# Performance work log

Measured on AMD Instinct MI355X. Metric: run time of the kernel, lower is better.

## Reference

```python
import jax, jax.numpy as jnp
import numpy as np

D = 512  # feature_dim


def setup_inputs() -> dict:
    key = jax.random.key(0)
    ks = jax.random.split(key, 10)
    s = 1.0 / np.sqrt(D)
    s2 = 1.0 / np.sqrt(2 * D)
    return {
        "X": jax.random.normal(ks[0], (8, 2048, D), dtype=jnp.float32),
        "Y": jax.random.normal(ks[1], (8, 2048, D), dtype=jnp.float32),
        "W_xq": jax.random.uniform(ks[2], (D, D), jnp.float32, -s, s),
        "b_xq": jax.random.uniform(ks[3], (D,), jnp.float32, -s, s),
        "W_yq": jax.random.uniform(ks[4], (D, D), jnp.float32, -s, s),
        "b_yq": jax.random.uniform(ks[5], (D,), jnp.float32, -s, s),
        "W_fk": jax.random.uniform(ks[6], (D, 2 * D), jnp.float32, -s2, s2),
        "b_fk": jax.random.uniform(ks[7], (D,), jnp.float32, -s2, s2),
        "W_fv": jax.random.uniform(ks[8], (D, 2 * D), jnp.float32, -s2, s2),
        "b_fv": jax.random.uniform(ks[9], (D,), jnp.float32, -s2, s2),
    }


def reference(X, Y, W_xq, b_xq, W_yq, b_yq, W_fk, b_fk, W_fv, b_fv):
    # Dropout is evaluated in eval mode (identity).
    scale = 1.0 / jnp.sqrt(jnp.asarray(D, X.dtype))
    Q1 = jnp.einsum('bsd,ed->bse', X, W_xq) + b_xq  # [B,S,D]
    Q2 = jnp.einsum('bsd,ed->bse', Y, W_yq) + b_yq
    Q_cat = jnp.concatenate([Q1, Q2], axis=-1)      # [B,S,2D]
    K_f = jnp.einsum('bsc,ec->bse', Q_cat, W_fk) + b_fk
    V_f = jnp.einsum('bsc,ec->bse', Q_cat, W_fv) + b_fv

    def attend(Q):
        scores = jnp.einsum('bqd,bkd->bqk', Q, K_f) * scale  # [B,S,S]
        A = jax.nn.softmax(scores, axis=-1)
        return jnp.einsum('bqk,bkd->bqd', A, V_f)

    U_A1 = X + attend(Q1)
    U_A2 = Y + attend(Q2)
    return U_A1 + U_A2
```

## Files before the change

kernel.cpp:

```cpp
#include <hip/hip_runtime.h>


#define B_    8
#define S_    2048
#define D_    512
#define M_TOT (B_ * S_)

typedef __bf16 bf16_t;
typedef __bf16 bf16x8 __attribute__((ext_vector_type(8)));
typedef __bf16 bf16x4 __attribute__((ext_vector_type(4)));
typedef float  f32x4  __attribute__((ext_vector_type(4)));

typedef __attribute__((address_space(1))) const void* gas_cv;
typedef __attribute__((address_space(3))) void*       las_v;

__device__ __forceinline__ f32x4 mfma16(bf16x8 a, bf16x8 b, f32x4 c) {
    return __builtin_amdgcn_mfma_f32_16x16x32_bf16(a, b, c, 0, 0, 0);
}
__device__ __forceinline__ void load_lds16(const void* g, void* l) {
    __builtin_amdgcn_global_load_lds((gas_cv)g, (las_v)l, 16, 0, 0);
}

__global__ __launch_bounds__(256) void k_cvt(
    const float* __restrict__ X, const float* __restrict__ Y,
    bf16_t* __restrict__ Xb, bf16_t* __restrict__ Yb)
{
    const int n4 = M_TOT * 512 / 4;
    for (int i = blockIdx.x * 256 + threadIdx.x; i < n4; i += 2048 * 256) {
        const float4 x = *(const float4*)(X + (size_t)i * 4);
        bf16x4 px = { (bf16_t)x.x, (bf16_t)x.y, (bf16_t)x.z, (bf16_t)x.w };
        *(bf16x4*)(Xb + (size_t)i * 4) = px;
        const float4 y = *(const float4*)(Y + (size_t)i * 4);
        bf16x4 py = { (bf16_t)y.x, (bf16_t)y.y, (bf16_t)y.z, (bf16_t)y.w };
        *(bf16x4*)(Yb + (size_t)i * 4) = py;
    }
}

__global__ __launch_bounds__(256) void k_qgemm(
    const float* __restrict__ X, const float* __restrict__ Y,
    const float* __restrict__ Wxq, const float* __restrict__ bxq,
    const float* __restrict__ Wyq, const float* __restrict__ byq,
    bf16_t* __restrict__ Qcat)
{
    __shared__ __attribute__((aligned(16))) bf16_t Al[128 * 40];
    __shared__ __attribute__((aligned(16))) bf16_t Bl[128 * 40];
    const int m0 = blockIdx.x * 128;
    const int n0 = blockIdx.y * 128;
    const bool second = (n0 >= 512);
    const float* A    = second ? Y : X;
    const float* W    = second ? Wyq : Wxq;
    const float* bias = second ? byq : bxq;
    const int nw = n0 & 511;
    const int t    = threadIdx.x;
    const int lane = t & 63;
    const int wv   = t >> 6;
    const int wm   = (wv & 1) * 64;
    const int wn   = (wv >> 1) * 64;
    const int l15  = lane & 15;
    const int quad = lane >> 4;

    f32x4 acc[4][4] = {};

    for (int k0 = 0; k0 < 512; k0 += 32) {
        __syncthreads();
#pragma unroll
        for (int p = 0; p < 4; ++p) {
            const int lin = p * 256 + t;
            const int row = lin >> 3;
            const int ch  = (lin & 7) * 4;
            const float4 va = *(const float4*)(A + (size_t)(m0 + row) * 512 + k0 + ch);
            bf16x4 pa = { (bf16_t)va.x, (bf16_t)va.y, (bf16_t)va.z, (bf16_t)va.w };
            *(bf16x4*)(Al + row * 40 + ch) = pa;
            const float4 vb = *(const float4*)(W + (size_t)(nw + row) * 512 + k0 + ch);
            bf16x4 pb = { (bf16_t)vb.x, (bf16_t)vb.y, (bf16_t)vb.z, (bf16_t)vb.w };
            *(bf16x4*)(Bl + row * 40 + ch) = pb;
        }
        __syncthreads();
        bf16x8 af[4], bfr[4];
#pragma unroll
        for (int i = 0; i < 4; ++i)
            af[i] = *(const bf16x8*)(Al + (wm + i * 16 + l15) * 40 + quad * 8);
#pragma unroll
        for (int i = 0; i < 4; ++i)
            bfr[i] = *(const bf16x8*)(Bl + (wn + i * 16 + l15) * 40 + quad * 8);
#pragma unroll
        for (int mt = 0; mt < 4; ++mt)
#pragma unroll
            for (int nt = 0; nt < 4; ++nt)
                acc[mt][nt] = mfma16(af[mt], bfr[nt], acc[mt][nt]);
    }

#pragma unroll
    for (int nt = 0; nt < 4; ++nt) {
        const int col  = n0 + wn + nt * 16 + l15;
        const float bv = bias[col & 511];
#pragma unroll
        for (int mt = 0; mt < 4; ++mt) {
            const int rowb = m0 + wm + mt * 16 + quad * 4;
#pragma unroll
            for (int r = 0; r < 4; ++r)
                Qcat[(size_t)(rowb + r) * 1024 + col] = (bf16_t)(acc[mt][nt][r] + bv);
        }
    }
}

__global__ __launch_bounds__(256) void k_qgemm_dma(
    const bf16_t* __restrict__ Xb, const bf16_t* __restrict__ Yb,
    const float* __restrict__ Wxq, const float* __restrict__ bxq,
    const float* __restrict__ Wyq, const float* __restrict__ byq,
    bf16_t* __restrict__ Qcat)
{
    __shared__ __attribute__((aligned(16))) bf16_t Al[128 * 32];
    __shared__ __attribute__((aligned(16))) bf16_t Bl[128 * 32];
    const int m0 = blockIdx.x * 128;
    const int n0 = blockIdx.y * 128;
    const bool second = (n0 >= 512);
    const bf16_t* A   = second ? Yb : Xb;
    const float* W    = second ? Wyq : Wxq;
    const float* bias = second ? byq : bxq;
    const int nw = n0 & 511;
    const int t    = threadIdx.x;
    const int lane = t & 63;
    const int wv   = t >> 6;
    const int wm   = (wv & 1) * 64;
    const int wn   = (wv >> 1) * 64;
    const int l15  = lane & 15;
    const int quad = lane >> 4;

    const int ar0 = t >> 2,          ac0 = (t & 3) * 8;
    const int ar1 = (256 + t) >> 2,  ac1 = ((256 + t) & 3) * 8;

    f32x4 acc[4][4] = {};

    for (int k0 = 0; k0 < 512; k0 += 32) {
        __syncthreads();
        load_lds16(A + (size_t)(m0 + ar0) * 512 + k0 + ac0, Al + t * 8);
        load_lds16(A + (size_t)(m0 + ar1) * 512 + k0 + ac1, Al + (256 + t) * 8);
#pragma unroll
        for (int p = 0; p < 4; ++p) {
            const int lin = p * 256 + t;
            const int row = lin >> 3;
            const int ch  = (lin & 7) * 4;
            const float4 vb = *(const float4*)(W + (size_t)(nw + row) * 512 + k0 + ch);
            bf16x4 pb = { (bf16_t)vb.x, (bf16_t)vb.y, (bf16_t)vb.z, (bf16_t)vb.w };
            *(bf16x4*)(Bl + row * 32 + ch) = pb;
        }
        __syncthreads();
        bf16x8 af[4], bfr[4];
#pragma unroll
        for (int i = 0; i < 4; ++i)
            af[i] = *(const bf16x8*)(Al + (wm + i * 16 + l15) * 32 + quad * 8);
#pragma unroll
        for (int i = 0; i < 4; ++i)
            bfr[i] = *(const bf16x8*)(Bl + (wn + i * 16 + l15) * 32 + quad * 8);
#pragma unroll
        for (int mt = 0; mt < 4; ++mt)
#pragma unroll
            for (int nt = 0; nt < 4; ++nt)
                acc[mt][nt] = mfma16(af[mt], bfr[nt], acc[mt][nt]);
    }

#pragma unroll
    for (int nt = 0; nt < 4; ++nt) {
        const int col  = n0 + wn + nt * 16 + l15;
        const float bv = bias[col & 511];
#pragma unroll
        for (int mt = 0; mt < 4; ++mt) {
            const int rowb = m0 + wm + mt * 16 + quad * 4;
#pragma unroll
            for (int r = 0; r < 4; ++r)
                Qcat[(size_t)(rowb + r) * 1024 + col] = (bf16_t)(acc[mt][nt][r] + bv);
        }
    }
}

__global__ __launch_bounds__(256) void k_kvgemm(
    const bf16_t* __restrict__ Qcat,
    const float* __restrict__ Wfk, const float* __restrict__ bfk,
    const float* __restrict__ Wfv, const float* __restrict__ bfv,
    bf16_t* __restrict__ Kf, bf16_t* __restrict__ Vt)
{
    __shared__ __attribute__((aligned(16))) union {
        struct { bf16_t Al[128 * 32]; bf16_t Bl[128 * 32]; } g;
        bf16_t T[128 * 132];
    } sm;
    const int m0 = blockIdx.x * 128;
    const int n0 = blockIdx.y * 128;
    const bool isV = (n0 >= 512);
    const float* W    = isV ? Wfv : Wfk;
    const float* bias = isV ? bfv : bfk;
    const int nw = n0 & 511;
    const int t    = threadIdx.x;
    const int lane = t & 63;
    const int wv   = t >> 6;
    const int wm   = (wv & 1) * 64;
    const int wn   = (wv >> 1) * 64;
    const int l15  = lane & 15;
    const int quad = lane >> 4;

    const int ar0 = t >> 2,          ac0 = (t & 3) * 8;
    const int ar1 = (256 + t) >> 2,  ac1 = ((256 + t) & 3) * 8;

    f32x4 acc[4][4] = {};

    for (int k0 = 0; k0 < 1024; k0 += 32) {
        __syncthreads();
        load_lds16(Qcat + (size_t)(m0 + ar0) * 1024 + k0 + ac0, sm.g.Al + t * 8);
        load_lds16(Qcat + (size_t)(m0 + ar1) * 1024 + k0 + ac1, sm.g.Al + (256 + t) * 8);
#pragma unroll
        for (int p = 0; p < 4; ++p) {
            const int lin = p * 256 + t;
            const int row = lin >> 3;
            const int ch  = (lin & 7) * 4;
            const float4 vb = *(const float4*)(W + (size_t)(nw + row) * 1024 + k0 + ch);
            bf16x4 pb = { (bf16_t)vb.x, (bf16_t)vb.y, (bf16_t)vb.z, (bf16_t)vb.w };
            *(bf16x4*)(sm.g.Bl + row * 32 + ch) = pb;
        }
        __syncthreads();
        bf16x8 af[4], bfr[4];
#pragma unroll
        for (int i = 0; i < 4; ++i)
            af[i] = *(const bf16x8*)(sm.g.Al + (wm + i * 16 + l15) * 32 + quad * 8);
#pragma unroll
        for (int i = 0; i < 4; ++i)
            bfr[i] = *(const bf16x8*)(sm.g.Bl + (wn + i * 16 + l15) * 32 + quad * 8);
#pragma unroll
        for (int mt = 0; mt < 4; ++mt)
#pragma unroll
            for (int nt = 0; nt < 4; ++nt)
                acc[mt][nt] = mfma16(af[mt], bfr[nt], acc[mt][nt]);
    }

    if (!isV) {
#pragma unroll
        for (int nt = 0; nt < 4; ++nt) {
            const int col  = n0 + wn + nt * 16 + l15;
            const float bv = bias[col];
#pragma unroll
            for (int mt = 0; mt < 4; ++mt) {
                const int rowb = m0 + wm + mt * 16 + quad * 4;
#pragma unroll
                for (int r = 0; r < 4; ++r)
                    Kf[(size_t)(rowb + r) * 512 + col] = (bf16_t)(acc[mt][nt][r] + bv);
            }
        }
    } else {
        __syncthreads();
#pragma unroll
        for (int nt = 0; nt < 4; ++nt) {
            const int dl = wn + nt * 16 + l15;
            const float bv = bias[nw + dl];
#pragma unroll
            for (int mt = 0; mt < 4; ++mt) {
                const int sl = wm + mt * 16 + quad * 4;
#pragma unroll
                for (int r = 0; r < 4; ++r)
                    sm.T[dl * 132 + sl + r] = (bf16_t)(acc[mt][nt][r] + bv);
            }
        }
        __syncthreads();
        const int bb = m0 >> 11;
        const int sb = m0 & 2047;
        const int half = lane >> 5;
        const int sl4  = (lane & 31) * 4;
#pragma unroll
        for (int i = 0; i < 16; ++i) {
            const int dl = wv * 32 + i * 2 + half;
            const bf16x4 v = *(const bf16x4*)(sm.T + dl * 132 + sl4);
            *(bf16x4*)(Vt + (size_t)(bb * 512 + nw + dl) * 2048 + sb + sl4) = v;
        }
    }
}

__global__ __launch_bounds__(256, 2) void k_attn(
    const bf16_t* __restrict__ Qcat, const bf16_t* __restrict__ Kf,
    const bf16_t* __restrict__ Vt,
    const float* __restrict__ X, const float* __restrict__ Y,
    float* __restrict__ out, bf16_t* __restrict__ attn,
    const int mode, const int which)
{
    __shared__ __attribute__((aligned(16))) bf16_t Kl[2][32 * 520];
    __shared__ __attribute__((aligned(16))) bf16_t Pl[2][64 * 36];
    __shared__ float lsumL[64];

    const int b = blockIdx.y;
    const int w = (mode == 0) ? (int)blockIdx.z : which;
    const int t    = threadIdx.x;
    const int lane = t & 63;
    const int wv   = t >> 6;
    const int l15  = lane & 15;
    const int quad = lane >> 4;
    const int q0   = blockIdx.x * 64;
    const int qw   = q0 + wv * 16;

    const bf16_t* Kbase = Kf + (size_t)b * S_ * 512;
    const bf16_t* Vbase = Vt + ((size_t)b * 512 + wv * 128) * S_;

    bf16x8 aq[16];
    {
        const bf16_t* qp = Qcat + (size_t)(b * S_ + qw + l15) * 1024 + w * 512 + quad * 8;
#pragma unroll
        for (int ks = 0; ks < 16; ++ks) aq[ks] = *(const bf16x8*)(qp + ks * 32);
    }

    f32x4 acc[4][8] = {};
    float lacc[4] = { 0.f, 0.f, 0.f, 0.f };
    const float sc2 = 0.04419417382415922f * 1.4426950408889634f;

#pragma unroll
    for (int p = 0; p < 8; ++p) {
        const int row = wv * 8 + p;
        load_lds16(Kbase + (size_t)row * 512 + lane * 8, Kl[0] + row * 520);
    }
    __syncthreads();

    {
#pragma unroll
        for (int p = 0; p < 8; ++p) {
            const int row = wv * 8 + p;
            load_lds16(Kbase + (size_t)(32 + row) * 512 + lane * 8, Kl[1] + row * 520);
        }
        f32x4 s0a = {}, s0b = {}, s1a = {}, s1b = {};
        __builtin_amdgcn_s_setprio(1);
#pragma unroll
        for (int ks = 0; ks < 16; ks += 2) {
            const bf16x8 b0 = *(const bf16x8*)(Kl[0] + l15 * 520 + ks * 32 + quad * 8);
            const bf16x8 b1 = *(const bf16x8*)(Kl[0] + (16 + l15) * 520 + ks * 32 + quad * 8);
            const bf16x8 c0 = *(const bf16x8*)(Kl[0] + l15 * 520 + (ks + 1) * 32 + quad * 8);
            const bf16x8 c1 = *(const bf16x8*)(Kl[0] + (16 + l15) * 520 + (ks + 1) * 32 + quad * 8);
            s0a = mfma16(aq[ks], b0, s0a);
            s1a = mfma16(aq[ks], b1, s1a);
            s0b = mfma16(aq[ks + 1], c0, s0b);
            s1b = mfma16(aq[ks + 1], c1, s1b);
        }
        __builtin_amdgcn_s_setprio(0);
        const f32x4 sA = s0a + s0b, sB = s1a + s1b;
#pragma unroll
        for (int r = 0; r < 4; ++r) {
            const float p0 = exp2f(sA[r] * sc2);
            const float p1 = exp2f(sB[r] * sc2);
            lacc[r] += p0 + p1;
            Pl[0][(wv * 16 + quad * 4 + r) * 36 + l15] = (bf16_t)p0;
            Pl[0][(wv * 16 + quad * 4 + r) * 36 + 16 + l15] = (bf16_t)p1;
        }
        __syncthreads();
    }

    for (int kb = 1; kb < 64; ++kb) {
        const int cur = kb & 1;
        const int prv = cur ^ 1;

        bf16x8 vb[8];
#pragma unroll
        for (int i = 0; i < 8; ++i)
            vb[i] = *(const bf16x8*)(Vbase + (size_t)(i * 16 + l15) * S_ +
                                     (kb - 1) * 32 + quad * 8);

        {
            const bf16_t* src = Kbase + (size_t)(kb + 1) * 32 * 512;
#pragma unroll
            for (int p = 0; p < 8; ++p) {
                const int row = wv * 8 + p;
                load_lds16(src + (size_t)row * 512 + lane * 8, Kl[prv] + row * 520);
            }
        }

        __builtin_amdgcn_s_setprio(1);
        f32x4 s0a = {}, s0b = {}, s1a = {}, s1b = {};
#pragma unroll
        for (int ks = 0; ks < 16; ks += 2) {
            const bf16x8 b0 = *(const bf16x8*)(Kl[cur] + l15 * 520 + ks * 32 + quad * 8);
            const bf16x8 b1 = *(const bf16x8*)(Kl[cur] + (16 + l15) * 520 + ks * 32 + quad * 8);
            const bf16x8 c0 = *(const bf16x8*)(Kl[cur] + l15 * 520 + (ks + 1) * 32 + quad * 8);
            const bf16x8 c1 = *(const bf16x8*)(Kl[cur] + (16 + l15) * 520 + (ks + 1) * 32 + quad * 8);
            s0a = mfma16(aq[ks], b0, s0a);
            s1a = mfma16(aq[ks], b1, s1a);
            s0b = mfma16(aq[ks + 1], c0, s0b);
            s1b = mfma16(aq[ks + 1], c1, s1b);
        }

        {
            bf16x8 ap[4];
#pragma unroll
            for (int qt = 0; qt < 4; ++qt) {
                const bf16x4 lo = *(const bf16x4*)(Pl[prv] + (qt * 16 + l15) * 36 + quad * 8);
                const bf16x4 hi = *(const bf16x4*)(Pl[prv] + (qt * 16 + l15) * 36 + quad * 8 + 4);
                ap[qt] = __builtin_shufflevector(lo, hi, 0, 1, 2, 3, 4, 5, 6, 7);
            }
#pragma unroll
            for (int dt = 0; dt < 8; ++dt)
#pragma unroll
                for (int qt = 0; qt < 4; ++qt)
                    acc[qt][dt] = mfma16(ap[qt], vb[dt], acc[qt][dt]);
        }
        __builtin_amdgcn_s_setprio(0);

        const f32x4 sA = s0a + s0b, sB = s1a + s1b;
#pragma unroll
        for (int r = 0; r < 4; ++r) {
            const float p0 = exp2f(sA[r] * sc2);
            const float p1 = exp2f(sB[r] * sc2);
            lacc[r] += p0 + p1;
            Pl[cur][(wv * 16 + quad * 4 + r) * 36 + l15] = (bf16_t)p0;
            Pl[cur][(wv * 16 + quad * 4 + r) * 36 + 16 + l15] = (bf16_t)p1;
        }

        __syncthreads();
    }

    {
        bf16x8 vb[8];
#pragma unroll
        for (int i = 0; i < 8; ++i)
            vb[i] = *(const bf16x8*)(Vbase + (size_t)(i * 16 + l15) * S_ +
                                     63 * 32 + quad * 8);
        bf16x8 ap[4];
#pragma unroll
        for (int qt = 0; qt < 4; ++qt) {
            const bf16x4 lo = *(const bf16x4*)(Pl[1] + (qt * 16 + l15) * 36 + quad * 8);
            const bf16x4 hi = *(const bf16x4*)(Pl[1] + (qt * 16 + l15) * 36 + quad * 8 + 4);
            ap[qt] = __builtin_shufflevector(lo, hi, 0, 1, 2, 3, 4, 5, 6, 7);
        }
#pragma unroll
        for (int dt = 0; dt < 8; ++dt)
#pragma unroll
            for (int qt = 0; qt < 4; ++qt)
                acc[qt][dt] = mfma16(ap[qt], vb[dt], acc[qt][dt]);
    }

    {
        float lrow[4];
#pragma unroll
        for (int r = 0; r < 4; ++r) {
            float v = lacc[r];
#pragma unroll
            for (int off = 1; off < 16; off <<= 1) v += __shfl_xor(v, off, 64);
            lrow[r] = v;
        }
        if (l15 == 0) {
#pragma unroll
            for (int r = 0; r < 4; ++r) lsumL[wv * 16 + quad * 4 + r] = lrow[r];
        }
    }
    __syncthreads();

#pragma unroll
    for (int qt = 0; qt < 4; ++qt) {
        f32x4 inv;
#pragma unroll
        for (int r = 0; r < 4; ++r) inv[r] = 1.0f / lsumL[qt * 16 + quad * 4 + r];
#pragma unroll
        for (int dt = 0; dt < 8; ++dt) {
            const int d = wv * 128 + dt * 16 + l15;
#pragma unroll
            for (int r = 0; r < 4; ++r) {
                const float v = acc[qt][dt][r] * inv[r];
                const size_t idx =
                    (size_t)(b * S_ + q0 + qt * 16 + quad * 4 + r) * 512 + d;
                if (mode == 0)      attn[(size_t)w * M_TOT * 512 + idx] = (bf16_t)v;
                else if (mode == 1) out[idx] = X[idx] + Y[idx] + v;
                else                out[idx] += v;
            }
        }
    }
}

__global__ __launch_bounds__(256) void k_add(
    const float* __restrict__ X, const float* __restrict__ Y,
    const bf16_t* __restrict__ a0, const bf16_t* __restrict__ a1,
    float* __restrict__ out)
{
    const size_t i = ((size_t)blockIdx.x * 256 + threadIdx.x) * 4;
    const float4 x = *(const float4*)(X + i);
    const float4 y = *(const float4*)(Y + i);
    const bf16x4 v0 = *(const bf16x4*)(a0 + i);
    const bf16x4 v1 = *(const bf16x4*)(a1 + i);
    float4 o;
    o.x = x.x + y.x + (float)v0[0] + (float)v1[0];
    o.y = x.y + y.y + (float)v0[1] + (float)v1[1];
    o.z = x.z + y.z + (float)v0[2] + (float)v1[2];
    o.w = x.w + y.w + (float)v0[3] + (float)v1[3];
    *(float4*)(out + i) = o;
}

extern "C" void kernel_launch(void* const* d_in, const int* in_sizes, int n_in,
                              void* d_out, int out_size, void* d_ws, size_t ws_size,
                              hipStream_t stream)
{
    const float* X   = (const float*)d_in[0];
    const float* Y   = (const float*)d_in[1];
    const float* Wxq = (const float*)d_in[2];
    const float* bxq = (const float*)d_in[3];
    const float* Wyq = (const float*)d_in[4];
    const float* byq = (const float*)d_in[5];
    const float* Wfk = (const float*)d_in[6];
    const float* bfk = (const float*)d_in[7];
    const float* Wfv = (const float*)d_in[8];
    const float* bfv = (const float*)d_in[9];
    float* out = (float*)d_out;
    char*  ws  = (char*)d_ws;

    bf16_t* Qcat = (bf16_t*)(ws);
    bf16_t* Kf   = (bf16_t*)(ws + (size_t)33554432);
    bf16_t* Vt   = (bf16_t*)(ws + (size_t)50331648);
    bf16_t* attn = (bf16_t*)(ws + (size_t)67108864);
    bf16_t* Xb   = (bf16_t*)(ws + (size_t)67108864);
    bf16_t* Yb   = (bf16_t*)(ws + (size_t)83886080);
    const bool big = ws_size >= (size_t)100663296;

    if (big) {
        k_cvt<<<dim3(2048), 256, 0, stream>>>(X, Y, Xb, Yb);
        k_qgemm_dma<<<dim3(128, 8), 256, 0, stream>>>(Xb, Yb, Wxq, bxq, Wyq, byq, Qcat);
    } else {
        k_qgemm<<<dim3(128, 8), 256, 0, stream>>>(X, Y, Wxq, bxq, Wyq, byq, Qcat);
    }
    k_kvgemm<<<dim3(128, 8), 256, 0, stream>>>(Qcat, Wfk, bfk, Wfv, bfv, Kf, Vt);
    if (big) {
        k_attn<<<dim3(32, 8, 2), 256, 0, stream>>>(Qcat, Kf, Vt, X, Y, out, attn, 0, 0);
        k_add<<<dim3(8192), 256, 0, stream>>>(X, Y, attn, attn + (size_t)M_TOT * 512, out);
    } else {
        k_attn<<<dim3(32, 8, 1), 256, 0, stream>>>(Qcat, Kf, Vt, X, Y, out, attn, 1, 0);
        k_attn<<<dim3(32, 8, 1), 256, 0, stream>>>(Qcat, Kf, Vt, X, Y, out, attn, 2, 1);
    }
}
```

Baseline: 529.1 us.

## Pre-convert weights to bf16, DMA both GEMM operands, fuse residual into attention

Adds a kernel that converts all four weight matrices to bf16 once per call, so both projection GEMMs can load A and B tiles straight into LDS with global_load_lds instead of converting fp32 weights in registers. In the attention kernel, the P tile row stride changes from 36 to 40 so P fragments load as single 16-byte reads. The setprio hints are removed. The first attention half now writes X+Y+attn directly to the output, and a lighter add kernel folds in only the second half, cutting one bf16 intermediate read and the X/Y reads. Workspace buffers are reused, with Yb aliasing Kf, which is safe only because of kernel ordering.

```diff
diff --git a/kernel.cpp b/kernel.cpp
--- a/kernel.cpp
+++ b/kernel.cpp
@@ -33,6 +33,176 @@
         const float4 y = *(const float4*)(Y + (size_t)i * 4);
         bf16x4 py = { (bf16_t)y.x, (bf16_t)y.y, (bf16_t)y.z, (bf16_t)y.w };
         *(bf16x4*)(Yb + (size_t)i * 4) = py;
+    }
+}
+
+__global__ __launch_bounds__(256) void k_cvtw(
+    const float* __restrict__ Wxq, const float* __restrict__ Wyq,
+    const float* __restrict__ Wfk, const float* __restrict__ Wfv,
+    bf16_t* __restrict__ Wb)
+{
+    const int j = blockIdx.x * 256 + threadIdx.x;
+    const float* src; int sj;
+    if (j < 65536)       { src = Wxq; sj = j; }
+    else if (j < 131072) { src = Wyq; sj = j - 65536; }
+    else if (j < 262144) { src = Wfk; sj = j - 131072; }
+    else                 { src = Wfv; sj = j - 262144; }
+    const float4 v = *(const float4*)(src + (size_t)sj * 4);
+    bf16x4 p = { (bf16_t)v.x, (bf16_t)v.y, (bf16_t)v.z, (bf16_t)v.w };
+    *(bf16x4*)(Wb + (size_t)j * 4) = p;
+}
+
+__global__ __launch_bounds__(256) void k_qgemm_bb(
+    const bf16_t* __restrict__ Xb, const bf16_t* __restrict__ Yb,
+    const bf16_t* __restrict__ Wb,
+    const float* __restrict__ bxq, const float* __restrict__ byq,
+    bf16_t* __restrict__ Qcat)
+{
+    __shared__ __attribute__((aligned(16))) bf16_t Al[128 * 32];
+    __shared__ __attribute__((aligned(16))) bf16_t Bl[128 * 32];
+    const int m0 = blockIdx.x * 128;
+    const int n0 = blockIdx.y * 128;
+    const bool second = (n0 >= 512);
+    const bf16_t* A   = second ? Yb : Xb;
+    const bf16_t* W   = Wb + (second ? 262144 : 0);
+    const float* bias = second ? byq : bxq;
+    const int nw = n0 & 511;
+    const int t    = threadIdx.x;
+    const int lane = t & 63;
+    const int wv   = t >> 6;
+    const int wm   = (wv & 1) * 64;
+    const int wn   = (wv >> 1) * 64;
+    const int l15  = lane & 15;
+    const int quad = lane >> 4;
+
+    const int ar0 = t >> 2,          ac0 = (t & 3) * 8;
+    const int ar1 = (256 + t) >> 2,  ac1 = ((256 + t) & 3) * 8;
+
+    f32x4 acc[4][4] = {};
+
+    for (int k0 = 0; k0 < 512; k0 += 32) {
+        __syncthreads();
+        load_lds16(A + (size_t)(m0 + ar0) * 512 + k0 + ac0, Al + t * 8);
+        load_lds16(A + (size_t)(m0 + ar1) * 512 + k0 + ac1, Al + (256 + t) * 8);
+        load_lds16(W + (size_t)(nw + ar0) * 512 + k0 + ac0, Bl + t * 8);
+        load_lds16(W + (size_t)(nw + ar1) * 512 + k0 + ac1, Bl + (256 + t) * 8);
+        __syncthreads();
+        bf16x8 af[4], bfr[4];
+#pragma unroll
+        for (int i = 0; i < 4; ++i)
+            af[i] = *(const bf16x8*)(Al + (wm + i * 16 + l15) * 32 + quad * 8);
+#pragma unroll
+        for (int i = 0; i < 4; ++i)
+            bfr[i] = *(const bf16x8*)(Bl + (wn + i * 16 + l15) * 32 + quad * 8);
+#pragma unroll
+        for (int mt = 0; mt < 4; ++mt)
+#pragma unroll
+            for (int nt = 0; nt < 4; ++nt)
+                acc[mt][nt] = mfma16(af[mt], bfr[nt], acc[mt][nt]);
+    }
+
+#pragma unroll
+    for (int nt = 0; nt < 4; ++nt) {
+        const int col  = n0 + wn + nt * 16 + l15;
+        const float bv = bias[col & 511];
+#pragma unroll
+        for (int mt = 0; mt < 4; ++mt) {
+            const int rowb = m0 + wm + mt * 16 + quad * 4;
+#pragma unroll
+            for (int r = 0; r < 4; ++r)
+                Qcat[(size_t)(rowb + r) * 1024 + col] = (bf16_t)(acc[mt][nt][r] + bv);
+        }
+    }
+}
+
+__global__ __launch_bounds__(256) void k_kvgemm_bb(
+    const bf16_t* __restrict__ Qcat,
+    const bf16_t* __restrict__ Wfkb, const float* __restrict__ bfk,
+    const bf16_t* __restrict__ Wfvb, const float* __restrict__ bfv,
+    bf16_t* __restrict__ Kf, bf16_t* __restrict__ Vt)
+{
+    __shared__ __attribute__((aligned(16))) union {
+        struct { bf16_t Al[128 * 32]; bf16_t Bl[128 * 32]; } g;
+        bf16_t T[128 * 132];
+    } sm;
+    const int m0 = blockIdx.x * 128;
+    const int n0 = blockIdx.y * 128;
+    const bool isV = (n0 >= 512);
+    const bf16_t* W   = isV ? Wfvb : Wfkb;
+    const float* bias = isV ? bfv : bfk;
+    const int nw = n0 & 511;
+    const int t    = threadIdx.x;
+    const int lane = t & 63;
+    const int wv   = t >> 6;
+    const int wm   = (wv & 1) * 64;
+    const int wn   = (wv >> 1) * 64;
+    const int l15  = lane & 15;
+    const int quad = lane >> 4;
+
+    const int ar0 = t >> 2,          ac0 = (t & 3) * 8;
+    const int ar1 = (256 + t) >> 2,  ac1 = ((256 + t) & 3) * 8;
+
+    f32x4 acc[4][4] = {};
+
+    for (int k0 = 0; k0 < 1024; k0 += 32) {
+        __syncthreads();
+        load_lds16(Qcat + (size_t)(m0 + ar0) * 1024 + k0 + ac0, sm.g.Al + t * 8);
+        load_lds16(Qcat + (size_t)(m0 + ar1) * 1024 + k0 + ac1, sm.g.Al + (256 + t) * 8);
+        load_lds16(W + (size_t)(nw + ar0) * 1024 + k0 + ac0, sm.g.Bl + t * 8);
+        load_lds16(W + (size_t)(nw + ar1) * 1024 + k0 + ac1, sm.g.Bl + (256 + t) * 8);
+        __syncthreads();
+        bf16x8 af[4], bfr[4];
+#pragma unroll
+        for (int i = 0; i < 4; ++i)
+            af[i] = *(const bf16x8*)(sm.g.Al + (wm + i * 16 + l15) * 32 + quad * 8);
+#pragma unroll
+        for (int i = 0; i < 4; ++i)
+            bfr[i] = *(const bf16x8*)(sm.g.Bl + (wn + i * 16 + l15) * 32 + quad * 8);
+#pragma unroll
+        for (int mt = 0; mt < 4; ++mt)
+#pragma unroll
+            for (int nt = 0; nt < 4; ++nt)
+                acc[mt][nt] = mfma16(af[mt], bfr[nt], acc[mt][nt]);
+    }
+
+    if (!isV) {
+#pragma unroll
+        for (int nt = 0; nt < 4; ++nt) {
+            const int col  = n0 + wn + nt * 16 + l15;
+            const float bv = bias[col];
+#pragma unroll
+            for (int mt = 0; mt < 4; ++mt) {
+                const int rowb = m0 + wm + mt * 16 + quad * 4;
+#pragma unroll
+                for (int r = 0; r < 4; ++r)
+                    Kf[(size_t)(rowb + r) * 512 + col] = (bf16_t)(acc[mt][nt][r] + bv);
+            }
+        }
+    } else {
+        __syncthreads();
+#pragma unroll
+        for (int nt = 0; nt < 4; ++nt) {
+            const int dl = wn + nt * 16 + l15;
+            const float bv = bias[nw + dl];
+#pragma unroll
+            for (int mt = 0; mt < 4; ++mt) {
+                const int sl = wm + mt * 16 + quad * 4;
+#pragma unroll
+                for (int r = 0; r < 4; ++r)
+                    sm.T[dl * 132 + sl + r] = (bf16_t)(acc[mt][nt][r] + bv);
+            }
+        }
+        __syncthreads();
+        const int bb = m0 >> 11;
+        const int sb = m0 & 2047;
+        const int half = lane >> 5;
+        const int sl4  = (lane & 31) * 4;
+#pragma unroll
+        for (int i = 0; i < 16; ++i) {
+            const int dl = wv * 32 + i * 2 + half;
+            const bf16x4 v = *(const bf16x4*)(sm.T + dl * 132 + sl4);
+            *(bf16x4*)(Vt + (size_t)(bb * 512 + nw + dl) * 2048 + sb + sl4) = v;
+        }
     }
 }
 
@@ -83,76 +253,6 @@
 #pragma unroll
         for (int i = 0; i < 4; ++i)
             bfr[i] = *(const bf16x8*)(Bl + (wn + i * 16 + l15) * 40 + quad * 8);
-#pragma unroll
-        for (int mt = 0; mt < 4; ++mt)
-#pragma unroll
-            for (int nt = 0; nt < 4; ++nt)
-                acc[mt][nt] = mfma16(af[mt], bfr[nt], acc[mt][nt]);
-    }
-
-#pragma unroll
-    for (int nt = 0; nt < 4; ++nt) {
-        const int col  = n0 + wn + nt * 16 + l15;
-        const float bv = bias[col & 511];
-#pragma unroll
-        for (int mt = 0; mt < 4; ++mt) {
-            const int rowb = m0 + wm + mt * 16 + quad * 4;
-#pragma unroll
-            for (int r = 0; r < 4; ++r)
-                Qcat[(size_t)(rowb + r) * 1024 + col] = (bf16_t)(acc[mt][nt][r] + bv);
-        }
-    }
-}
-
-__global__ __launch_bounds__(256) void k_qgemm_dma(
-    const bf16_t* __restrict__ Xb, const bf16_t* __restrict__ Yb,
-    const float* __restrict__ Wxq, const float* __restrict__ bxq,
-    const float* __restrict__ Wyq, const float* __restrict__ byq,
-    bf16_t* __restrict__ Qcat)
-{
-    __shared__ __attribute__((aligned(16))) bf16_t Al[128 * 32];
-    __shared__ __attribute__((aligned(16))) bf16_t Bl[128 * 32];
-    const int m0 = blockIdx.x * 128;
-    const int n0 = blockIdx.y * 128;
-    const bool second = (n0 >= 512);
-    const bf16_t* A   = second ? Yb : Xb;
-    const float* W    = second ? Wyq : Wxq;
-    const float* bias = second ? byq : bxq;
-    const int nw = n0 & 511;
-    const int t    = threadIdx.x;
-    const int lane = t & 63;
-    const int wv   = t >> 6;
-    const int wm   = (wv & 1) * 64;
-    const int wn   = (wv >> 1) * 64;
-    const int l15  = lane & 15;
-    const int quad = lane >> 4;
-
-    const int ar0 = t >> 2,          ac0 = (t & 3) * 8;
-    const int ar1 = (256 + t) >> 2,  ac1 = ((256 + t) & 3) * 8;
-
-    f32x4 acc[4][4] = {};
-
-    for (int k0 = 0; k0 < 512; k0 += 32) {
-        __syncthreads();
-        load_lds16(A + (size_t)(m0 + ar0) * 512 + k0 + ac0, Al + t * 8);
-        load_lds16(A + (size_t)(m0 + ar1) * 512 + k0 + ac1, Al + (256 + t) * 8);
-#pragma unroll
-        for (int p = 0; p < 4; ++p) {
-            const int lin = p * 256 + t;
-            const int row = lin >> 3;
-            const int ch  = (lin & 7) * 4;
-            const float4 vb = *(const float4*)(W + (size_t)(nw + row) * 512 + k0 + ch);
-            bf16x4 pb = { (bf16_t)vb.x, (bf16_t)vb.y, (bf16_t)vb.z, (bf16_t)vb.w };
-            *(bf16x4*)(Bl + row * 32 + ch) = pb;
-        }
-        __syncthreads();
-        bf16x8 af[4], bfr[4];
-#pragma unroll
-        for (int i = 0; i < 4; ++i)
-            af[i] = *(const bf16x8*)(Al + (wm + i * 16 + l15) * 32 + quad * 8);
-#pragma unroll
-        for (int i = 0; i < 4; ++i)
-            bfr[i] = *(const bf16x8*)(Bl + (wn + i * 16 + l15) * 32 + quad * 8);
 #pragma unroll
         for (int mt = 0; mt < 4; ++mt)
 #pragma unroll
@@ -280,11 +380,11 @@
     const int mode, const int which)
 {
     __shared__ __attribute__((aligned(16))) bf16_t Kl[2][32 * 520];
-    __shared__ __attribute__((aligned(16))) bf16_t Pl[2][64 * 36];
+    __shared__ __attribute__((aligned(16))) bf16_t Pl[2][64 * 40];
     __shared__ float lsumL[64];
 
     const int b = blockIdx.y;
-    const int w = (mode == 0) ? (int)blockIdx.z : which;
+    const int w = (mode == 1 || mode == 2) ? which : (int)blockIdx.z;
     const int t    = threadIdx.x;
     const int lane = t & 63;
     const int wv   = t >> 6;
@@ -321,7 +421,6 @@
             load_lds16(Kbase + (size_t)(32 + row) * 512 + lane * 8, Kl[1] + row * 520);
         }
         f32x4 s0a = {}, s0b = {}, s1a = {}, s1b = {};
-        __builtin_amdgcn_s_setprio(1);
 #pragma unroll
         for (int ks = 0; ks < 16; ks += 2) {
             const bf16x8 b0 = *(const bf16x8*)(Kl[0] + l15 * 520 + ks * 32 + quad * 8);
@@ -333,15 +432,14 @@
             s0b = mfma16(aq[ks + 1], c0, s0b);
             s1b = mfma16(aq[ks + 1], c1, s1b);
         }
-        __builtin_amdgcn_s_setprio(0);
         const f32x4 sA = s0a + s0b, sB = s1a + s1b;
 #pragma unroll
         for (int r = 0; r < 4; ++r) {
             const float p0 = exp2f(sA[r] * sc2);
             const float p1 = exp2f(sB[r] * sc2);
             lacc[r] += p0 + p1;
-            Pl[0][(wv * 16 + quad * 4 + r) * 36 + l15] = (bf16_t)p0;
-            Pl[0][(wv * 16 + quad * 4 + r) * 36 + 16 + l15] = (bf16_t)p1;
+            Pl[0][(wv * 16 + quad * 4 + r) * 40 + l15] = (bf16_t)p0;
+            Pl[0][(wv * 16 + quad * 4 + r) * 40 + 16 + l15] = (bf16_t)p1;
         }
         __syncthreads();
     }
@@ -365,7 +463,6 @@
             }
         }
 
-        __builtin_amdgcn_s_setprio(1);
         f32x4 s0a = {}, s0b = {}, s1a = {}, s1b = {};
 #pragma unroll
         for (int ks = 0; ks < 16; ks += 2) {
@@ -382,18 +479,14 @@
         {
             bf16x8 ap[4];
 #pragma unroll
-            for (int qt = 0; qt < 4; ++qt) {
-                const bf16x4 lo = *(const bf16x4*)(Pl[prv] + (qt * 16 + l15) * 36 + quad * 8);
-                const bf16x4 hi = *(const bf16x4*)(Pl[prv] + (qt * 16 + l15) * 36 + quad * 8 + 4);
-                ap[qt] = __builtin_shufflevector(lo, hi, 0, 1, 2, 3, 4, 5, 6, 7);
-            }
+            for (int qt = 0; qt < 4; ++qt)
+                ap[qt] = *(const bf16x8*)(Pl[prv] + (qt * 16 + l15) * 40 + quad * 8);
 #pragma unroll
             for (int dt = 0; dt < 8; ++dt)
 #pragma unroll
                 for (int qt = 0; qt < 4; ++qt)
                     acc[qt][dt] = mfma16(ap[qt], vb[dt], acc[qt][dt]);
         }
-        __builtin_amdgcn_s_setprio(0);
 
         const f32x4 sA = s0a + s0b, sB = s1a + s1b;
 #pragma unroll
@@ -401,8 +494,8 @@
             const float p0 = exp2f(sA[r] * sc2);
             const float p1 = exp2f(sB[r] * sc2);
             lacc[r] += p0 + p1;
-            Pl[cur][(wv * 16 + quad * 4 + r) * 36 + l15] = (bf16_t)p0;
-            Pl[cur][(wv * 16 + quad * 4 + r) * 36 + 16 + l15] = (bf16_t)p1;
+            Pl[cur][(wv * 16 + quad * 4 + r) * 40 + l15] = (bf16_t)p0;
+            Pl[cur][(wv * 16 + quad * 4 + r) * 40 + 16 + l15] = (bf16_t)p1;
         }
 
         __syncthreads();
@@ -416,11 +509,8 @@
                                      63 * 32 + quad * 8);
         bf16x8 ap[4];
 #pragma unroll
-        for (int qt = 0; qt < 4; ++qt) {
-            const bf16x4 lo = *(const bf16x4*)(Pl[1] + (qt * 16 + l15) * 36 + quad * 8);
-            const bf16x4 hi = *(const bf16x4*)(Pl[1] + (qt * 16 + l15) * 36 + quad * 8 + 4);
-            ap[qt] = __builtin_shufflevector(lo, hi, 0, 1, 2, 3, 4, 5, 6, 7);
-        }
+        for (int qt = 0; qt < 4; ++qt)
+            ap[qt] = *(const bf16x8*)(Pl[1] + (qt * 16 + l15) * 40 + quad * 8);
 #pragma unroll
         for (int dt = 0; dt < 8; ++dt)
 #pragma unroll
@@ -457,29 +547,31 @@
                 const float v = acc[qt][dt][r] * inv[r];
                 const size_t idx =
                     (size_t)(b * S_ + q0 + qt * 16 + quad * 4 + r) * 512 + d;
-                if (mode == 0)      attn[(size_t)w * M_TOT * 512 + idx] = (bf16_t)v;
-                else if (mode == 1) out[idx] = X[idx] + Y[idx] + v;
-                else                out[idx] += v;
+                if (mode == 3) {
+                    if (w == 0) out[idx] = X[idx] + Y[idx] + v;
+                    else        attn[idx] = (bf16_t)v;
+                } else if (mode == 0) {
+                    attn[(size_t)w * M_TOT * 512 + idx] = (bf16_t)v;
+                } else if (mode == 1) {
+                    out[idx] = X[idx] + Y[idx] + v;
+                } else {
+                    out[idx] += v;
+                }
             }
         }
     }
 }
 
-__global__ __launch_bounds__(256) void k_add(
-    const float* __restrict__ X, const float* __restrict__ Y,
-    const bf16_t* __restrict__ a0, const bf16_t* __restrict__ a1,
-    float* __restrict__ out)
+__global__ __launch_bounds__(256) void k_add2(
+    const bf16_t* __restrict__ a1, float* __restrict__ out)
 {
     const size_t i = ((size_t)blockIdx.x * 256 + threadIdx.x) * 4;
-    const float4 x = *(const float4*)(X + i);
-    const float4 y = *(const float4*)(Y + i);
-    const bf16x4 v0 = *(const bf16x4*)(a0 + i);
+    float4 o = *(const float4*)(out + i);
     const bf16x4 v1 = *(const bf16x4*)(a1 + i);
-    float4 o;
-    o.x = x.x + y.x + (float)v0[0] + (float)v1[0];
-    o.y = x.y + y.y + (float)v0[1] + (float)v1[1];
-    o.z = x.z + y.z + (float)v0[2] + (float)v1[2];
-    o.w = x.w + y.w + (float)v0[3] + (float)v1[3];
+    o.x += (float)v1[0];
+    o.y += (float)v1[1];
+    o.z += (float)v1[2];
+    o.w += (float)v1[3];
     *(float4*)(out + i) = o;
 }
 
@@ -503,23 +595,24 @@
     bf16_t* Qcat = (bf16_t*)(ws);
     bf16_t* Kf   = (bf16_t*)(ws + (size_t)33554432);
     bf16_t* Vt   = (bf16_t*)(ws + (size_t)50331648);
-    bf16_t* attn = (bf16_t*)(ws + (size_t)67108864);
-    bf16_t* Xb   = (bf16_t*)(ws + (size_t)67108864);
-    bf16_t* Yb   = (bf16_t*)(ws + (size_t)83886080);
+    bf16_t* Wb   = (bf16_t*)(ws + (size_t)67108864);
+    bf16_t* at1  = (bf16_t*)(ws + (size_t)67108864);
+    bf16_t* Xb   = (bf16_t*)(ws + (size_t)83886080);
+    bf16_t* Yb   = Kf;
     const bool big = ws_size >= (size_t)100663296;
 
     if (big) {
         k_cvt<<<dim3(2048), 256, 0, stream>>>(X, Y, Xb, Yb);
-        k_qgemm_dma<<<dim3(128, 8), 256, 0, stream>>>(Xb, Yb, Wxq, bxq, Wyq, byq, Qcat);
+        k_cvtw<<<dim3(1536), 256, 0, stream>>>(Wxq, Wyq, Wfk, Wfv, Wb);
+        k_qgemm_bb<<<dim3(128, 8), 256, 0, stream>>>(Xb, Yb, Wb, bxq, byq, Qcat);
+        k_kvgemm_bb<<<dim3(128, 8), 256, 0, stream>>>(Qcat, Wb + 524288, bfk,
+                                                      Wb + 1048576, bfv, Kf, Vt);
+        k_attn<<<dim3(32, 8, 2), 256, 0, stream>>>(Qcat, Kf, Vt, X, Y, out, at1, 3, 0);
+        k_add2<<<dim3(8192), 256, 0, stream>>>(at1, out);
     } else {
         k_qgemm<<<dim3(128, 8), 256, 0, stream>>>(X, Y, Wxq, bxq, Wyq, byq, Qcat);
-    }
-    k_kvgemm<<<dim3(128, 8), 256, 0, stream>>>(Qcat, Wfk, bfk, Wfv, bfv, Kf, Vt);
-    if (big) {
-        k_attn<<<dim3(32, 8, 2), 256, 0, stream>>>(Qcat, Kf, Vt, X, Y, out, attn, 0, 0);
-        k_add<<<dim3(8192), 256, 0, stream>>>(X, Y, attn, attn + (size_t)M_TOT * 512, out);
-    } else {
-        k_attn<<<dim3(32, 8, 1), 256, 0, stream>>>(Qcat, Kf, Vt, X, Y, out, attn, 1, 0);
-        k_attn<<<dim3(32, 8, 1), 256, 0, stream>>>(Qcat, Kf, Vt, X, Y, out, attn, 2, 1);
-    }
-}
+        k_kvgemm<<<dim3(128, 8), 256, 0, stream>>>(Qcat, Wfk, bfk, Wfv, bfv, Kf, Vt);
+        k_attn<<<dim3(32, 8, 1), 256, 0, stream>>>(Qcat, Kf, Vt, X, Y, out, at1, 1, 0);
+        k_attn<<<dim3(32, 8, 1), 256, 0, stream>>>(Qcat, Kf, Vt, X, Y, out, at1, 2, 1);
+    }
+}
```

Measured after the change: 471.1 us. -11.0%, faster.
